# Kernel optimization log

Measured on AMD Instinct MI355X. Metric: run time of the kernel, lower is better.

The kernel has to match this reference:

```python
import jax, jax.numpy as jnp
import numpy as np
import math

D = 768; H = 12; DH = 64; LAT = 512; B = 2; L = 1024


def _rms(x, w, eps=1e-6):
    return w * x * jax.lax.rsqrt(jnp.mean(x * x, axis=-1, keepdims=True) + eps)


def _rope_tables(seq_len, dh):
    inv = 1.0 / (10000.0 ** (np.arange(0, dh, 2, dtype=np.float32) / dh))
    t = np.arange(seq_len, dtype=np.float32)
    f = np.outer(t, inv)
    emb = np.concatenate([f, f], axis=-1)
    return jnp.asarray(np.cos(emb))[None, :, None, :], jnp.asarray(np.sin(emb))[None, :, None, :]


def _rope(x, cos, sin):
    x1, x2 = jnp.split(x, 2, axis=-1)
    return x * cos + jnp.concatenate([-x2, x1], axis=-1) * sin


def setup_inputs():
    key = jax.random.key(0)
    ks = jax.random.split(key, 8)
    s = 0.02
    return {
        'x': jax.random.normal(ks[0], (B, L, D), jnp.float32),
        'w_ln': jnp.ones((D,), jnp.float32),
        'w_compress': jax.random.normal(ks[1], (D, LAT), jnp.float32) * s,
        'w_qkv': jax.random.normal(ks[2], (LAT, 3 * D), jnp.float32) * s,
        'w_reso': jax.random.normal(ks[3], (LAT, H * 4), jnp.float32) * s,
        'w_qn': jnp.ones((DH,), jnp.float32),
        'w_kn': jnp.ones((DH,), jnp.float32),
        'head_decay': jnp.linspace(-3.0, 1.0, H).astype(jnp.float32),
        'temperature': jnp.ones((1,), jnp.float32) * 0.5,
        'w_out_gate': jax.random.normal(ks[4], (LAT, D), jnp.float32) * s,
        'w_proj': jax.random.normal(ks[5], (D, D), jnp.float32) * s,
        'w_memnorm': jnp.ones((D,), jnp.float32),
    }


def reference(x, w_ln, w_compress, w_qkv, w_reso, w_qn, w_kn, head_decay, temperature, w_out_gate, w_proj, w_memnorm):
    cos, sin = _rope_tables(L, DH)
    xn = _rms(x, w_ln)
    latent = jax.nn.silu(xn @ w_compress)                        # (B,L,LAT)
    q, k, v = jnp.split(latent @ w_qkv, 3, axis=-1)
    q = _rope(_rms(q.reshape(B, L, H, DH), w_qn), cos, sin)
    k = _rope(_rms(k.reshape(B, L, H, DH), w_kn), cos, sin)
    v_f = v.reshape(B, L, H, DH)
    q_f = jax.nn.elu(q) + 1.0
    k_f = jax.nn.elu(k) + 1.0
    params = (latent @ w_reso).reshape(B, L, H, 4)
    sem_amp, sem_phase, ctx_amp, ctx_phase = [params[..., i] for i in range(4)]
    sem_phase = jax.nn.sigmoid(sem_phase) * math.pi
    ctx_phase = jax.nn.sigmoid(ctx_phase) * math.pi
    decay = jnp.clip(0.3 + 0.65 * jax.nn.sigmoid(head_decay), 1e-5, 0.999)   # (H,)
    gate = jnp.clip(jax.nn.sigmoid(jax.nn.sigmoid(sem_amp) * jax.nn.sigmoid(ctx_amp)
                                   * jnp.cos(sem_phase - ctx_phase) * temperature[0]) * 1.2 - 0.1,
                    0.05, 0.95)                                  # (B,L,H)
    one_m = (1.0 - decay)[None, None, :]                          # (1,1,H)
    kv_in = jnp.einsum('blhd,blhe->blhde', k_f, v_f) * gate[..., None, None] * one_m[..., None, None]
    z_in = k_f * one_m[..., None]
    # cumulative log-decay -> df, same as torch cumsum of constant per-step log_decay
    cum_log = jnp.arange(1, L + 1, dtype=jnp.float32)[:, None] * jnp.log(decay)[None, :]
    df = jnp.exp(cum_log)[None, :, :, None]                       # (1,L,H,1)
    kv_states = jnp.cumsum(kv_in / (df[..., None] + 1e-8), axis=1) * df[..., None]
    z_states = jnp.cumsum(z_in / (df + 1e-8), axis=1) * df
    out_num = jnp.einsum('blhd,blhde->blhe', q_f, kv_states)
    den = jnp.clip(jnp.sum(q_f * z_states, axis=-1, keepdims=True), 1e-5, None)
    out = (out_num / den).reshape(B, L, D)
    return (_rms(out, w_memnorm) @ w_proj) * jax.nn.silu(latent @ w_out_gate)
```

## Files before the change

kernel.cpp:

```cpp
#include <hip/hip_runtime.h>
#include <hip/hip_bf16.h>
#include <math.h>

#define D_MODEL 768
#define NHEAD   12
#define LATD    512
#define BATCH   2
#define SEQ     1024
#define NROWS   (BATCH*SEQ)
#define NCHUNK  (SEQ/64)
#define NBH     (BATCH*NHEAD)
#define NFUSE   3200
#define PQ      72

using short8 = __attribute__((ext_vector_type(8))) short;
using f32x4  = __attribute__((ext_vector_type(4))) float;

__device__ __forceinline__ float sigf(float x){ return 1.f/(1.f+expf(-x)); }
__device__ __forceinline__ float decay_of(float hd){
  float d = 0.3f + 0.65f*sigf(hd);
  return fminf(fmaxf(d, 1e-5f), 0.999f);
}
__device__ __forceinline__ unsigned short f2b(float f){
  __hip_bfloat16 h = __float2bfloat16(f);
  return *reinterpret_cast<unsigned short*>(&h);
}
__device__ __forceinline__ float bf2f(unsigned short u){
  unsigned int x = ((unsigned int)u) << 16;
  return __uint_as_float(x);
}
__device__ __forceinline__ void async16(const unsigned short* g, unsigned short* l){
  __builtin_amdgcn_global_load_lds((const __attribute__((address_space(1))) void*)g,
                                   (__attribute__((address_space(3))) void*)l, 16, 0, 0);
}

__global__ __launch_bounds__(256) void k_rmsnorm_bf(const float* __restrict__ x,
    const float* __restrict__ w, unsigned short* __restrict__ y)
{
  int row = blockIdx.x, tid = threadIdx.x;
  const float* xr = x + (size_t)row*D_MODEL;
  float v0 = xr[tid], v1 = xr[tid+256], v2 = xr[tid+512];
  float s = v0*v0 + v1*v1 + v2*v2;
  #pragma unroll
  for (int off=32; off; off>>=1) s += __shfl_xor(s, off, 64);
  __shared__ float red[4];
  if ((tid & 63) == 0) red[tid>>6] = s;
  __syncthreads();
  s = red[0]+red[1]+red[2]+red[3];
  float sc = rsqrtf(s*(1.f/(float)D_MODEL) + 1e-6f);
  unsigned short* yr = y + (size_t)row*D_MODEL;
  yr[tid]     = f2b(v0*sc*w[tid]);
  yr[tid+256] = f2b(v1*sc*w[tid+256]);
  yr[tid+512] = f2b(v2*sc*w[tid+512]);
}

__global__ __launch_bounds__(256) void k_cvt_all(const float* __restrict__ wc,
    const float* __restrict__ wq, const float* __restrict__ wr,
    const float* __restrict__ wg, const float* __restrict__ wp,
    unsigned short* __restrict__ wtc, unsigned short* __restrict__ wtq,
    unsigned short* __restrict__ wtg, unsigned short* __restrict__ wtp)
{
  __shared__ unsigned short tile[64][65];
  int blk = blockIdx.x, t = threadIdx.x;
  const float* W; unsigned short* WT; int K, N, bx, by;
  if (blk < 96){ W=wc; WT=wtc; K=768; N=512; bx=blk&7; by=blk>>3; }
  else if (blk < 384){ int i=blk-96;  W=wq; WT=wtq; K=512; N=2304; bx=i%36; by=i/36; }
  else if (blk < 480){ int i=blk-384; W=wg; WT=wtg; K=512; N=768;  bx=i%12; by=i/12; }
  else if (blk < 624){ int i=blk-480; W=wp; WT=wtp; K=768; N=768;  bx=i%12; by=i/12; }
  else {
    int i = blk - 624;
    #pragma unroll
    for (int j=0;j<16;j++){
      int e = i*4096 + t + j*256;
      int n = 2304 + (e >> 9), k = e & 511;
      float v = (n < 2352) ? wr[(size_t)k*48 + (n-2304)] : 0.f;
      wtq[(size_t)n*512 + k] = f2b(v);
    }
    return;
  }
  int k0 = by*64, n0 = bx*64, cr = t >> 6, cc = t & 63;
  #pragma unroll
  for (int i=0;i<16;i++){
    int r = cr + i*4;
    tile[r][cc] = f2b(W[(size_t)(k0+r)*N + n0 + cc]);
  }
  __syncthreads();
  #pragma unroll
  for (int i=0;i<16;i++){
    int nn = cr + i*4;
    WT[(size_t)(n0+nn)*K + k0 + cc] = tile[cc][nn];
  }
}

__global__ __launch_bounds__(256) void k_mfma_gemm(const unsigned short* __restrict__ A,
    const unsigned short* __restrict__ BT, float* __restrict__ Cf,
    unsigned short* __restrict__ Cb, const unsigned short* __restrict__ auxb,
    int M, int N, int K, int act)
{
  __shared__ unsigned short As[128*64];
  __shared__ unsigned short Bs[128*64];
  int tid = threadIdx.x;
  int w = tid >> 6, lane = tid & 63;
  int wm = (w >> 1)*64, wn = (w & 1)*64;
  int m16 = lane & 15, quad = lane >> 4;
  int bm = blockIdx.y*128, bn = blockIdx.x*128;

  f32x4 acc[4][4];
  #pragma unroll
  for (int i=0;i<4;i++)
    #pragma unroll
    for (int j=0;j<4;j++) acc[i][j] = (f32x4){0.f,0.f,0.f,0.f};

  for (int kk = 0; kk < K; kk += 64){
    #pragma unroll
    for (int i=0;i<4;i++){
      int g = (w*4 + i)*64 + lane;
      int m = g >> 3, c = (g & 7) ^ (m & 7);
      async16(A  + (size_t)(bm+m)*K + kk + c*8, As + (w*4+i)*512);
      async16(BT + (size_t)(bn+m)*K + kk + c*8, Bs + (w*4+i)*512);
    }
    __syncthreads();
    #pragma unroll
    for (int s=0;s<2;s++){
      short8 af[4], bf[4];
      #pragma unroll
      for (int mt=0;mt<4;mt++){
        int m = wm + mt*16 + m16;
        int idx = m*8 + ((s*4 + quad) ^ (m & 7));
        af[mt] = *(const short8*)(As + idx*8);
      }
      #pragma unroll
      for (int nt=0;nt<4;nt++){
        int n = wn + nt*16 + m16;
        int idx = n*8 + ((s*4 + quad) ^ (n & 7));
        bf[nt] = *(const short8*)(Bs + idx*8);
      }
      #pragma unroll
      for (int mt=0;mt<4;mt++)
        #pragma unroll
        for (int nt=0;nt<4;nt++)
          acc[mt][nt] = __builtin_amdgcn_mfma_f32_16x16x32_bf16(af[mt], bf[nt], acc[mt][nt], 0, 0, 0);
    }
    __syncthreads();
  }
  #pragma unroll
  for (int mt=0;mt<4;mt++){
    #pragma unroll
    for (int r=0;r<4;r++){
      int row = bm + wm + mt*16 + quad*4 + r;
      #pragma unroll
      for (int nt=0;nt<4;nt++){
        int col = bn + wn + nt*16 + m16;
        float v = acc[mt][nt][r];
        if (act == 1) v = v/(1.f + __expf(-v));
        else if (act == 2) v *= bf2f(auxb[(size_t)row*N + col]);
        if (Cf) Cf[(size_t)row*N + col] = v;
        if (Cb) Cb[(size_t)row*N + col] = f2b(v);
      }
    }
  }
}

__global__ __launch_bounds__(256) void k_gemm_fused(const unsigned short* __restrict__ A,
    const unsigned short* __restrict__ BT, const float* __restrict__ w_qn,
    const float* __restrict__ w_kn, unsigned short* __restrict__ qf,
    unsigned short* __restrict__ kf, unsigned short* __restrict__ vf,
    float* __restrict__ params, unsigned short* __restrict__ gateb)
{
  __shared__ unsigned short As[128*64];
  __shared__ unsigned short Bs[128*64];
  const int K = LATD, N = NFUSE;
  int tid = threadIdx.x;
  int w = tid >> 6, lane = tid & 63;
  int wm = (w >> 1)*64, wn = (w & 1)*64;
  int m16 = lane & 15, quad = lane >> 4;
  int bm = blockIdx.y*128, bn = blockIdx.x*128;

  f32x4 acc[4][4];
  #pragma unroll
  for (int i=0;i<4;i++)
    #pragma unroll
    for (int j=0;j<4;j++) acc[i][j] = (f32x4){0.f,0.f,0.f,0.f};

  for (int kk = 0; kk < K; kk += 64){
    #pragma unroll
    for (int i=0;i<4;i++){
      int g = (w*4 + i)*64 + lane;
      int m = g >> 3, c = (g & 7) ^ (m & 7);
      async16(A  + (size_t)(bm+m)*K + kk + c*8, As + (w*4+i)*512);
      async16(BT + (size_t)(bn+m)*K + kk + c*8, Bs + (w*4+i)*512);
    }
    __syncthreads();
    #pragma unroll
    for (int s=0;s<2;s++){
      short8 af[4], bf[4];
      #pragma unroll
      for (int mt=0;mt<4;mt++){
        int m = wm + mt*16 + m16;
        int idx = m*8 + ((s*4 + quad) ^ (m & 7));
        af[mt] = *(const short8*)(As + idx*8);
      }
      #pragma unroll
      for (int nt=0;nt<4;nt++){
        int n = wn + nt*16 + m16;
        int idx = n*8 + ((s*4 + quad) ^ (n & 7));
        bf[nt] = *(const short8*)(Bs + idx*8);
      }
      #pragma unroll
      for (int mt=0;mt<4;mt++)
        #pragma unroll
        for (int nt=0;nt<4;nt++)
          acc[mt][nt] = __builtin_amdgcn_mfma_f32_16x16x32_bf16(af[mt], bf[nt], acc[mt][nt], 0, 0, 0);
    }
    __syncthreads();
  }

  int colbase = bn + wn;
  if (colbase < 2304){
    int sec = colbase >= 1536 ? 2 : (colbase >= 768 ? 1 : 0);
    int h = (colbase - sec*768) >> 6;
    if (sec == 2){
      #pragma unroll
      for (int mt=0;mt<4;mt++)
        #pragma unroll
        for (int r=0;r<4;r++){
          int row = bm + wm + mt*16 + quad*4 + r;
          int b = row >> 10, t = row & 1023;
          size_t ob = (((size_t)(b*NHEAD+h))*SEQ + t)*64;
          #pragma unroll
          for (int nt=0;nt<4;nt++)
            vf[ob + nt*16 + m16] = f2b(acc[mt][nt][r]);
        }
    } else {
      const float* wnp = sec ? w_kn : w_qn;
      unsigned short* of = sec ? kf : qf;
      float wv4[4];
      #pragma unroll
      for (int nt=0;nt<4;nt++) wv4[nt] = wnp[nt*16 + m16];
      float inv0 = exp2f(-(float)m16*(1.f/32.f)*13.28771237954945f);
      float inv1 = inv0 * 0.01f;
      #pragma unroll
      for (int mt=0;mt<4;mt++)
        #pragma unroll
        for (int r=0;r<4;r++){
          int row = bm + wm + mt*16 + quad*4 + r;
          int b = row >> 10, t = row & 1023;
          float s = 0.f;
          #pragma unroll
          for (int nt=0;nt<4;nt++) s += acc[mt][nt][r]*acc[mt][nt][r];
          s += __shfl_xor(s, 1, 64); s += __shfl_xor(s, 2, 64);
          s += __shfl_xor(s, 4, 64); s += __shfl_xor(s, 8, 64);
          float rs = rsqrtf(s*(1.f/64.f) + 1e-6f);
          float qv[4];
          #pragma unroll
          for (int nt=0;nt<4;nt++) qv[nt] = acc[mt][nt][r]*rs*wv4[nt];
          float s0,c0,s1,c1;
          __sincosf((float)t*inv0, &s0, &c0);
          __sincosf((float)t*inv1, &s1, &c1);
          size_t ob = (((size_t)(b*NHEAD+h))*SEQ + t)*64;
          #pragma unroll
          for (int nt=0;nt<4;nt++){
            float rot = (nt < 2) ? -qv[nt+2] : qv[nt-2];
            float cs = (nt & 1) ? c1 : c0, sn = (nt & 1) ? s1 : s0;
            float val = qv[nt]*cs + rot*sn;
            val = (val > 0.f) ? val + 1.f : __expf(val);
            of[ob + nt*16 + m16] = f2b(val);
          }
        }
    }
  } else if (colbase < 2432){
    #pragma unroll
    for (int mt=0;mt<4;mt++)
      #pragma unroll
      for (int r=0;r<4;r++){
        int row = bm + wm + mt*16 + quad*4 + r;
        #pragma unroll
        for (int nt=0;nt<4;nt++){
          int p = colbase + nt*16 + m16 - 2304;
          if (p < 48) params[(size_t)row*48 + p] = acc[mt][nt][r];
        }
      }
  } else {
    #pragma unroll
    for (int mt=0;mt<4;mt++)
      #pragma unroll
      for (int r=0;r<4;r++){
        int row = bm + wm + mt*16 + quad*4 + r;
        #pragma unroll
        for (int nt=0;nt<4;nt++){
          int gc = colbase + nt*16 + m16 - 2432;
          float v = acc[mt][nt][r];
          v = v/(1.f + __expf(-v));
          gateb[(size_t)row*D_MODEL + gc] = f2b(v);
        }
      }
  }
}

__global__ __launch_bounds__(256) void k_coef(const float* __restrict__ params,
    const float* __restrict__ hdec, const float* __restrict__ temp,
    float* __restrict__ cKV, float* __restrict__ cG)
{
  int idx = blockIdx.x*256 + threadIdx.x;
  int row = idx / NHEAD, h = idx % NHEAD;
  int b = row >> 10, t = row & 1023;
  const float* pr = params + (size_t)row*48 + h*4;
  float sa = sigf(pr[0]);
  float sp = sigf(pr[1])*3.14159265358979323846f;
  float ca = sigf(pr[2]);
  float cp = sigf(pr[3])*3.14159265358979323846f;
  float z = sa*ca*cosf(sp - cp)*temp[0];
  float gate = fminf(fmaxf(sigf(z)*1.2f - 0.1f, 0.05f), 0.95f);
  float d = decay_of(hdec[h]);
  float df = expf((float)(t+1)*logf(d));
  float g = df/(df + 1e-8f);
  int ci = (b*NHEAD + h)*SEQ + t;
  cKV[ci] = g*gate*(1.f - d);
  cG[ci]  = 1.f/gate;
}

__global__ __launch_bounds__(256) void k_intra(const unsigned short* __restrict__ qf,
    const unsigned short* __restrict__ kf, const unsigned short* __restrict__ vf,
    const float* __restrict__ cKVb, const float* __restrict__ cGb,
    const float* __restrict__ hdec, float* __restrict__ numb,
    float* __restrict__ denb, float* __restrict__ Pb, float* __restrict__ zPb)
{
  __shared__ __align__(16) unsigned short Qb[64*PQ];
  __shared__ __align__(16) unsigned short Kb[64*PQ];
  __shared__ __align__(16) unsigned short KtS[64*PQ];
  __shared__ __align__(16) unsigned short Wb[64*PQ];
  __shared__ __align__(16) unsigned short Vt[80*PQ];
  __shared__ float cn[64], cps[64];
  int bid = blockIdx.x;
  int chunk = bid & 15, bh = bid >> 4, h = bh % NHEAD;
  int tid = threadIdx.x, w = tid >> 6, lane = tid & 63;
  int m16 = lane & 15, quad = lane >> 4;
  size_t base = ((size_t)bh*SEQ + chunk*64)*64;
  float d = decay_of(hdec[h]);
  float l2d = log2f(d);

  if (tid < 64){
    float c = cKVb[bh*SEQ + chunk*64 + tid];
    float pw = exp2f((float)(63 - tid)*l2d);
    cn[tid] = c;
    cps[tid] = c*pw;
    Vt[64*PQ + tid] = f2b(cGb[bh*SEQ + chunk*64 + tid]);
  }
  for (int i = tid; i < 15*PQ; i += 256) Vt[65*PQ + i] = 0;
  __syncthreads();

  #pragma unroll
  for (int i=0;i<2;i++){
    int g = tid + i*256;
    int r = g >> 3, c8 = (g & 7)*8;
    *(short8*)(Qb + r*PQ + c8) = *(const short8*)(qf + base + r*64 + c8);
    *(short8*)(Kb + r*PQ + c8) = *(const short8*)(kf + base + r*64 + c8);
  }
  {
    int s = tid & 63;
    float cpss = cps[s];
    #pragma unroll
    for (int i=0;i<2;i++){
      int c8 = ((tid >> 6) + i*4)*8;
      short8 vv = *(const short8*)(vf + base + s*64 + c8);
      short8 kk = *(const short8*)(kf + base + s*64 + c8);
      #pragma unroll
      for (int j=0;j<8;j++){
        Vt[(c8+j)*PQ + s] = ((unsigned short*)&vv)[j];
        KtS[(c8+j)*PQ + s] = f2b(bf2f(((unsigned short*)&kk)[j])*cpss);
      }
    }
  }
  __syncthreads();

  int trow = w*16 + quad*4;
  for (int stile=0; stile<4; stile++){
    if (stile > w){
      #pragma unroll
      for (int r=0;r<4;r++) Wb[(trow+r)*PQ + stile*16 + m16] = 0;
      continue;
    }
    f32x4 acc = (f32x4){0.f,0.f,0.f,0.f};
    #pragma unroll
    for (int ks=0;ks<2;ks++){
      short8 a = *(const short8*)(Qb + (w*16 + m16)*PQ + ks*32 + quad*8);
      short8 b = *(const short8*)(Kb + (stile*16 + m16)*PQ + ks*32 + quad*8);
      acc = __builtin_amdgcn_mfma_f32_16x16x32_bf16(a, b, acc, 0, 0, 0);
    }
    int s = stile*16 + m16;
    float cns = cn[s];
    #pragma unroll
    for (int r=0;r<4;r++){
      int t = trow + r;
      float wv = 0.f;
      if (s <= t) wv = acc[r]*exp2f((float)(t-s)*l2d)*cns;
      Wb[t*PQ + s] = f2b(wv);
    }
  }
  __syncthreads();

  {
    f32x4 acc[5];
    #pragma unroll
    for (int et=0;et<5;et++) acc[et] = (f32x4){0.f,0.f,0.f,0.f};
    #pragma unroll
    for (int et=0;et<5;et++)
      #pragma unroll
      for (int ks=0;ks<2;ks++){
        short8 a = *(const short8*)(Wb + (w*16 + m16)*PQ + ks*32 + quad*8);
        short8 b = *(const short8*)(Vt + (et*16 + m16)*PQ + ks*32 + quad*8);
        acc[et] = __builtin_amdgcn_mfma_f32_16x16x32_bf16(a, b, acc[et], 0, 0, 0);
      }
    #pragma unroll
    for (int et=0;et<4;et++)
      #pragma unroll
      for (int r=0;r<4;r++)
        numb[base + (size_t)(trow+r)*64 + et*16 + m16] = acc[et][r];
    if (m16 == 0){
      #pragma unroll
      for (int r=0;r<4;r++)
        denb[bh*SEQ + chunk*64 + trow + r] = acc[4][r];
    }
  }
  {
    #pragma unroll
    for (int j=0;j<5;j++){
      int tIdx = w + 4*j;
      int et = tIdx >> 2, dt = tIdx & 3;
      f32x4 acc = (f32x4){0.f,0.f,0.f,0.f};
      #pragma unroll
      for (int ks=0;ks<2;ks++){
        short8 a = *(const short8*)(Vt  + (et*16 + m16)*PQ + ks*32 + quad*8);
        short8 b = *(const short8*)(KtS + (dt*16 + m16)*PQ + ks*32 + quad*8);
        acc = __builtin_amdgcn_mfma_f32_16x16x32_bf16(a, b, acc, 0, 0, 0);
      }
      if (et < 4){
        #pragma unroll
        for (int r=0;r<4;r++)
          Pb[(size_t)bid*4096 + (et*16 + quad*4 + r)*64 + dt*16 + m16] = acc[r];
      } else {
        if (quad == 0) zPb[bid*64 + dt*16 + m16] = acc[0];
      }
    }
  }
}

__global__ __launch_bounds__(256) void k_scan(const float* __restrict__ Pb,
    const float* __restrict__ zPb, unsigned short* __restrict__ Sprev,
    unsigned short* __restrict__ zprev, const float* __restrict__ hdec)
{
  int bh = blockIdx.x >> 2, part = blockIdx.x & 3;
  int h = bh % NHEAD, tid = threadIdx.x;
  float d = decay_of(hdec[h]);
  float d64 = exp2f(64.f*log2f(d));
  int idx = part*1024 + tid*4;
  float4 S = make_float4(0.f,0.f,0.f,0.f);
  for (int c=0;c<NCHUNK;c++){
    size_t off = ((size_t)bh*NCHUNK + c)*4096 + idx;
    unsigned int lo = (unsigned int)f2b(S.x) | ((unsigned int)f2b(S.y) << 16);
    unsigned int hi = (unsigned int)f2b(S.z) | ((unsigned int)f2b(S.w) << 16);
    *(uint2*)(Sprev + off) = make_uint2(lo, hi);
    float4 p = *(const float4*)(Pb + off);
    S.x = S.x*d64 + p.x; S.y = S.y*d64 + p.y;
    S.z = S.z*d64 + p.z; S.w = S.w*d64 + p.w;
  }
  if (part == 0 && tid < 64){
    float z = 0.f;
    for (int c=0;c<NCHUNK;c++){
      int zoff = (bh*NCHUNK + c)*64 + tid;
      zprev[zoff] = f2b(z);
      z = z*d64 + zPb[zoff];
    }
  }
}

__global__ __launch_bounds__(256) void k_cross(const unsigned short* __restrict__ qf,
    const unsigned short* __restrict__ Sprev, const unsigned short* __restrict__ zprev,
    const float* __restrict__ numb, const float* __restrict__ denb,
    const float* __restrict__ hdec, float* __restrict__ attn)
{
  __shared__ __align__(16) unsigned short Qb[64*PQ];
  __shared__ __align__(16) unsigned short Sp[80*PQ];
  __shared__ float den_sm[64];
  int bid = blockIdx.x;
  int chunk = bid & 15, bh = bid >> 4, h = bh % NHEAD, b = bh / NHEAD;
  int tid = threadIdx.x, w = tid >> 6, lane = tid & 63;
  int m16 = lane & 15, quad = lane >> 4;
  size_t base = ((size_t)bh*SEQ + chunk*64)*64;
  float d = decay_of(hdec[h]);
  float l2d = log2f(d);

  #pragma unroll
  for (int i=0;i<2;i++){
    int g = tid + i*256;
    int r = g >> 3, c8 = (g & 7)*8;
    *(short8*)(Qb + r*PQ + c8) = *(const short8*)(qf + base + r*64 + c8);
    *(short8*)(Sp + r*PQ + c8) = *(const short8*)(Sprev + (size_t)bid*4096 + r*64 + c8);
  }
  if (tid < 64) Sp[64*PQ + tid] = zprev[bid*64 + tid];
  for (int i = tid; i < 15*PQ; i += 256) Sp[65*PQ + i] = 0;
  __syncthreads();

  f32x4 acc[5];
  #pragma unroll
  for (int et=0;et<5;et++) acc[et] = (f32x4){0.f,0.f,0.f,0.f};
  #pragma unroll
  for (int et=0;et<5;et++)
    #pragma unroll
    for (int ks=0;ks<2;ks++){
      short8 a = *(const short8*)(Qb + (w*16 + m16)*PQ + ks*32 + quad*8);
      short8 b = *(const short8*)(Sp + (et*16 + m16)*PQ + ks*32 + quad*8);
      acc[et] = __builtin_amdgcn_mfma_f32_16x16x32_bf16(a, b, acc[et], 0, 0, 0);
    }
  int trow = w*16 + quad*4;
  if (m16 == 0){
    #pragma unroll
    for (int r=0;r<4;r++){
      int tl = trow + r;
      float pw = exp2f((float)(tl+1)*l2d);
      float den = fmaxf(denb[bh*SEQ + chunk*64 + tl] + pw*acc[4][r], 1e-5f);
      den_sm[tl] = 1.f/den;
    }
  }
  __syncthreads();
  #pragma unroll
  for (int r=0;r<4;r++){
    int tl = trow + r;
    float pw = exp2f((float)(tl+1)*l2d);
    float invden = den_sm[tl];
    int tg = chunk*64 + tl;
    #pragma unroll
    for (int et=0;et<4;et++){
      int e = et*16 + m16;
      float nm = numb[base + (size_t)tl*64 + e] + pw*acc[et][r];
      attn[((size_t)(b*SEQ + tg))*D_MODEL + h*64 + e] = nm*invden;
    }
  }
}

extern "C" void kernel_launch(void* const* d_in, const int* in_sizes, int n_in,
                              void* d_out, int out_size, void* d_ws, size_t ws_size,
                              hipStream_t stream)
{
  (void)in_sizes; (void)n_in; (void)out_size; (void)ws_size;
  const float* x       = (const float*)d_in[0];
  const float* w_ln    = (const float*)d_in[1];
  const float* w_comp  = (const float*)d_in[2];
  const float* w_qkv   = (const float*)d_in[3];
  const float* w_reso  = (const float*)d_in[4];
  const float* w_qn    = (const float*)d_in[5];
  const float* w_kn    = (const float*)d_in[6];
  const float* hdec    = (const float*)d_in[7];
  const float* temp    = (const float*)d_in[8];
  const float* w_ogate = (const float*)d_in[9];
  const float* w_proj  = (const float*)d_in[10];
  const float* w_mn    = (const float*)d_in[11];
  float* ws = (float*)d_ws;
  float* out = (float*)d_out;

  const size_t o_params = 0;
  const size_t o_cKV    = o_params + (size_t)NROWS*48;
  const size_t o_cG     = o_cKV    + (size_t)NBH*SEQ;
  const size_t o_den    = o_cG     + (size_t)NBH*SEQ;
  const size_t o_P      = o_den    + (size_t)NBH*SEQ;
  const size_t o_zP     = o_P      + (size_t)NBH*NCHUNK*4096;
  const size_t o_attn   = o_zP     + (size_t)NBH*NCHUNK*64;
  const size_t o_numb   = o_attn   + (size_t)NROWS*D_MODEL;
  const size_t o_end    = o_numb   + (size_t)NBH*SEQ*64;

  unsigned short* bws = (unsigned short*)(ws + o_end);
  const size_t u_xn     = 0;
  const size_t u_latent = u_xn     + (size_t)NROWS*D_MODEL;
  const size_t u_memn   = u_latent + (size_t)NROWS*LATD;
  const size_t u_q      = u_memn   + (size_t)NROWS*D_MODEL;
  const size_t u_k      = u_q      + (size_t)NBH*SEQ*64;
  const size_t u_v      = u_k      + (size_t)NBH*SEQ*64;
  const size_t u_gate   = u_v      + (size_t)NBH*SEQ*64;
  const size_t u_S      = u_gate   + (size_t)NROWS*D_MODEL;
  const size_t u_zprev  = u_S      + (size_t)NBH*NCHUNK*4096;
  const size_t u_wtc    = u_zprev  + (size_t)NBH*NCHUNK*64;
  const size_t u_wtq    = u_wtc    + (size_t)LATD*D_MODEL;
  const size_t u_wtg    = u_wtq    + (size_t)2432*LATD;
  const size_t u_wtp    = u_wtg    + (size_t)D_MODEL*LATD;

  k_cvt_all<<<640, 256, 0, stream>>>(w_comp, w_qkv, w_reso, w_ogate, w_proj,
      bws + u_wtc, bws + u_wtq, bws + u_wtg, bws + u_wtp);
  k_rmsnorm_bf<<<NROWS, 256, 0, stream>>>(x, w_ln, bws + u_xn);
  k_mfma_gemm<<<dim3(LATD/128, NROWS/128), 256, 0, stream>>>(bws + u_xn, bws + u_wtc,
      nullptr, bws + u_latent, nullptr, NROWS, LATD, D_MODEL, 1);
  k_gemm_fused<<<dim3(NFUSE/128, NROWS/128), 256, 0, stream>>>(bws + u_latent, bws + u_wtq,
      w_qn, w_kn, bws + u_q, bws + u_k, bws + u_v, ws + o_params, bws + u_gate);
  k_coef<<<NROWS*NHEAD/256, 256, 0, stream>>>(ws + o_params, hdec, temp, ws + o_cKV, ws + o_cG);
  k_intra<<<NBH*NCHUNK, 256, 0, stream>>>(bws + u_q, bws + u_k, bws + u_v,
      ws + o_cKV, ws + o_cG, hdec, ws + o_numb, ws + o_den, ws + o_P, ws + o_zP);
  k_scan<<<NBH*4, 256, 0, stream>>>(ws + o_P, ws + o_zP, bws + u_S, bws + u_zprev, hdec);
  k_cross<<<NBH*NCHUNK, 256, 0, stream>>>(bws + u_q, bws + u_S, bws + u_zprev,
      ws + o_numb, ws + o_den, hdec, ws + o_attn);
  k_rmsnorm_bf<<<NROWS, 256, 0, stream>>>(ws + o_attn, w_mn, bws + u_memn);
  k_mfma_gemm<<<dim3(D_MODEL/128, NROWS/128), 256, 0, stream>>>(bws + u_memn, bws + u_wtp,
      out, nullptr, bws + u_gate, NROWS, D_MODEL, D_MODEL, 2);
}
```

Baseline: 182.7 us.

## Fuse attention stages into cooperative kernel and fold norms and coefficients into neighbors

Merges the intra-chunk, scan, cross-chunk and output RMSnorm stages into one cooperative kernel separated by grid-wide syncs. The gate and decay coefficient math moves into the fused QKV GEMM epilogue, and the input RMSnorm joins the weight-convert launch. The generic GEMM tile is narrowed to 128x64 so more blocks cover the small GEMMs. This cuts launch count and intermediate traffic, but grid.sync barriers and a scan phase using only 96 of 384 blocks serialize some work.

```diff
diff --git a/kernel.cpp b/kernel.cpp
--- a/kernel.cpp
+++ b/kernel.cpp
@@ -1,6 +1,9 @@
 #include <hip/hip_runtime.h>
 #include <hip/hip_bf16.h>
+#include <hip/hip_cooperative_groups.h>
 #include <math.h>
+
+namespace cg = cooperative_groups;
 
 #define D_MODEL 768
 #define NHEAD   12
@@ -12,6 +15,7 @@
 #define NBH     (BATCH*NHEAD)
 #define NFUSE   3200
 #define PQ      72
+#define NATTN   (NBH*NCHUNK)
 
 using short8 = __attribute__((ext_vector_type(8))) short;
 using f32x4  = __attribute__((ext_vector_type(4))) float;
@@ -34,40 +38,35 @@
                                    (__attribute__((address_space(3))) void*)l, 16, 0, 0);
 }
 
-__global__ __launch_bounds__(256) void k_rmsnorm_bf(const float* __restrict__ x,
-    const float* __restrict__ w, unsigned short* __restrict__ y)
-{
-  int row = blockIdx.x, tid = threadIdx.x;
-  const float* xr = x + (size_t)row*D_MODEL;
-  float v0 = xr[tid], v1 = xr[tid+256], v2 = xr[tid+512];
-  float s = v0*v0 + v1*v1 + v2*v2;
-  #pragma unroll
-  for (int off=32; off; off>>=1) s += __shfl_xor(s, off, 64);
-  __shared__ float red[4];
-  if ((tid & 63) == 0) red[tid>>6] = s;
-  __syncthreads();
-  s = red[0]+red[1]+red[2]+red[3];
-  float sc = rsqrtf(s*(1.f/(float)D_MODEL) + 1e-6f);
-  unsigned short* yr = y + (size_t)row*D_MODEL;
-  yr[tid]     = f2b(v0*sc*w[tid]);
-  yr[tid+256] = f2b(v1*sc*w[tid+256]);
-  yr[tid+512] = f2b(v2*sc*w[tid+512]);
-}
-
 __global__ __launch_bounds__(256) void k_cvt_all(const float* __restrict__ wc,
     const float* __restrict__ wq, const float* __restrict__ wr,
     const float* __restrict__ wg, const float* __restrict__ wp,
+    const float* __restrict__ x, const float* __restrict__ wln,
     unsigned short* __restrict__ wtc, unsigned short* __restrict__ wtq,
-    unsigned short* __restrict__ wtg, unsigned short* __restrict__ wtp)
+    unsigned short* __restrict__ wtg, unsigned short* __restrict__ wtp,
+    unsigned short* __restrict__ xn)
 {
   __shared__ unsigned short tile[64][65];
+  __shared__ float red[4];
   int blk = blockIdx.x, t = threadIdx.x;
-  const float* W; unsigned short* WT; int K, N, bx, by;
-  if (blk < 96){ W=wc; WT=wtc; K=768; N=512; bx=blk&7; by=blk>>3; }
-  else if (blk < 384){ int i=blk-96;  W=wq; WT=wtq; K=512; N=2304; bx=i%36; by=i/36; }
-  else if (blk < 480){ int i=blk-384; W=wg; WT=wtg; K=512; N=768;  bx=i%12; by=i/12; }
-  else if (blk < 624){ int i=blk-480; W=wp; WT=wtp; K=768; N=768;  bx=i%12; by=i/12; }
-  else {
+  if (blk >= 640){
+    int row = blk - 640;
+    const float* xr = x + (size_t)row*D_MODEL;
+    float v0 = xr[t], v1 = xr[t+256], v2 = xr[t+512];
+    float s = v0*v0 + v1*v1 + v2*v2;
+    #pragma unroll
+    for (int off=32; off; off>>=1) s += __shfl_xor(s, off, 64);
+    if ((t & 63) == 0) red[t>>6] = s;
+    __syncthreads();
+    s = red[0]+red[1]+red[2]+red[3];
+    float sc = rsqrtf(s*(1.f/(float)D_MODEL) + 1e-6f);
+    unsigned short* yr = xn + (size_t)row*D_MODEL;
+    yr[t]     = f2b(v0*sc*wln[t]);
+    yr[t+256] = f2b(v1*sc*wln[t+256]);
+    yr[t+512] = f2b(v2*sc*wln[t+512]);
+    return;
+  }
+  if (blk >= 624){
     int i = blk - 624;
     #pragma unroll
     for (int j=0;j<16;j++){
@@ -78,6 +77,11 @@
     }
     return;
   }
+  const float* W; unsigned short* WT; int K, N, bx, by;
+  if (blk < 96){ W=wc; WT=wtc; K=768; N=512; bx=blk&7; by=blk>>3; }
+  else if (blk < 384){ int i=blk-96;  W=wq; WT=wtq; K=512; N=2304; bx=i%36; by=i/36; }
+  else if (blk < 480){ int i=blk-384; W=wg; WT=wtg; K=512; N=768;  bx=i%12; by=i/12; }
+  else               { int i=blk-480; W=wp; WT=wtp; K=768; N=768;  bx=i%12; by=i/12; }
   int k0 = by*64, n0 = bx*64, cr = t >> 6, cc = t & 63;
   #pragma unroll
   for (int i=0;i<16;i++){
@@ -98,31 +102,36 @@
     int M, int N, int K, int act)
 {
   __shared__ unsigned short As[128*64];
-  __shared__ unsigned short Bs[128*64];
+  __shared__ unsigned short Bs[64*64];
   int tid = threadIdx.x;
   int w = tid >> 6, lane = tid & 63;
-  int wm = (w >> 1)*64, wn = (w & 1)*64;
+  int wm = (w >> 1)*64, wn = (w & 1)*32;
   int m16 = lane & 15, quad = lane >> 4;
-  int bm = blockIdx.y*128, bn = blockIdx.x*128;
-
-  f32x4 acc[4][4];
+  int bm = blockIdx.y*128, bn = blockIdx.x*64;
+
+  f32x4 acc[4][2];
   #pragma unroll
   for (int i=0;i<4;i++)
     #pragma unroll
-    for (int j=0;j<4;j++) acc[i][j] = (f32x4){0.f,0.f,0.f,0.f};
+    for (int j=0;j<2;j++) acc[i][j] = (f32x4){0.f,0.f,0.f,0.f};
 
   for (int kk = 0; kk < K; kk += 64){
     #pragma unroll
     for (int i=0;i<4;i++){
       int g = (w*4 + i)*64 + lane;
       int m = g >> 3, c = (g & 7) ^ (m & 7);
-      async16(A  + (size_t)(bm+m)*K + kk + c*8, As + (w*4+i)*512);
-      async16(BT + (size_t)(bn+m)*K + kk + c*8, Bs + (w*4+i)*512);
+      async16(A + (size_t)(bm+m)*K + kk + c*8, As + (w*4+i)*512);
+    }
+    #pragma unroll
+    for (int i=0;i<2;i++){
+      int g = (w*2 + i)*64 + lane;
+      int m = g >> 3, c = (g & 7) ^ (m & 7);
+      async16(BT + (size_t)(bn+m)*K + kk + c*8, Bs + (w*2+i)*512);
     }
     __syncthreads();
     #pragma unroll
     for (int s=0;s<2;s++){
-      short8 af[4], bf[4];
+      short8 af[4], bf[2];
       #pragma unroll
       for (int mt=0;mt<4;mt++){
         int m = wm + mt*16 + m16;
@@ -130,7 +139,7 @@
         af[mt] = *(const short8*)(As + idx*8);
       }
       #pragma unroll
-      for (int nt=0;nt<4;nt++){
+      for (int nt=0;nt<2;nt++){
         int n = wn + nt*16 + m16;
         int idx = n*8 + ((s*4 + quad) ^ (n & 7));
         bf[nt] = *(const short8*)(Bs + idx*8);
@@ -138,7 +147,7 @@
       #pragma unroll
       for (int mt=0;mt<4;mt++)
         #pragma unroll
-        for (int nt=0;nt<4;nt++)
+        for (int nt=0;nt<2;nt++)
           acc[mt][nt] = __builtin_amdgcn_mfma_f32_16x16x32_bf16(af[mt], bf[nt], acc[mt][nt], 0, 0, 0);
     }
     __syncthreads();
@@ -149,7 +158,7 @@
     for (int r=0;r<4;r++){
       int row = bm + wm + mt*16 + quad*4 + r;
       #pragma unroll
-      for (int nt=0;nt<4;nt++){
+      for (int nt=0;nt<2;nt++){
         int col = bn + wn + nt*16 + m16;
         float v = acc[mt][nt][r];
         if (act == 1) v = v/(1.f + __expf(-v));
@@ -163,13 +172,15 @@
 
 __global__ __launch_bounds__(256) void k_gemm_fused(const unsigned short* __restrict__ A,
     const unsigned short* __restrict__ BT, const float* __restrict__ w_qn,
-    const float* __restrict__ w_kn, unsigned short* __restrict__ qf,
+    const float* __restrict__ w_kn, const float* __restrict__ hdec,
+    const float* __restrict__ temp, unsigned short* __restrict__ qf,
     unsigned short* __restrict__ kf, unsigned short* __restrict__ vf,
-    float* __restrict__ params, unsigned short* __restrict__ gateb)
+    float* __restrict__ cKV, float* __restrict__ cG,
+    unsigned short* __restrict__ gateb)
 {
   __shared__ unsigned short As[128*64];
   __shared__ unsigned short Bs[128*64];
-  const int K = LATD, N = NFUSE;
+  const int K = LATD;
   int tid = threadIdx.x;
   int w = tid >> 6, lane = tid & 63;
   int wm = (w >> 1)*64, wn = (w & 1)*64;
@@ -268,19 +279,38 @@
           }
         }
     }
-  } else if (colbase < 2432){
+  } else if (colbase == 2304){
+    float temp0 = temp[0];
     #pragma unroll
     for (int mt=0;mt<4;mt++)
       #pragma unroll
       for (int r=0;r<4;r++){
         int row = bm + wm + mt*16 + quad*4 + r;
-        #pragma unroll
-        for (int nt=0;nt<4;nt++){
-          int p = colbase + nt*16 + m16 - 2304;
-          if (p < 48) params[(size_t)row*48 + p] = acc[mt][nt][r];
-        }
-      }
-  } else {
+        int b = row >> 10, t = row & 1023;
+        #pragma unroll
+        for (int nt=0;nt<3;nt++){
+          int p = nt*16 + m16, h2 = p >> 2, pi = p & 3;
+          float v  = acc[mt][nt][r];
+          float v1 = __shfl_xor(v, 1, 64);
+          float v2 = __shfl_xor(v, 2, 64);
+          float v3 = __shfl_xor(v, 3, 64);
+          if (pi == 0){
+            float sa = sigf(v);
+            float sp = sigf(v1)*3.14159265358979323846f;
+            float ca = sigf(v2);
+            float cp = sigf(v3)*3.14159265358979323846f;
+            float z = sa*ca*cosf(sp - cp)*temp0;
+            float gate = fminf(fmaxf(sigf(z)*1.2f - 0.1f, 0.05f), 0.95f);
+            float dd = decay_of(hdec[h2]);
+            float df = expf((float)(t+1)*logf(dd));
+            float g = df/(df + 1e-8f);
+            int ci = (b*NHEAD + h2)*SEQ + t;
+            cKV[ci] = g*gate*(1.f - dd);
+            cG[ci]  = 1.f/gate;
+          }
+        }
+      }
+  } else if (colbase >= 2432){
     #pragma unroll
     for (int mt=0;mt<4;mt++)
       #pragma unroll
@@ -297,191 +327,19 @@
   }
 }
 
-__global__ __launch_bounds__(256) void k_coef(const float* __restrict__ params,
-    const float* __restrict__ hdec, const float* __restrict__ temp,
-    float* __restrict__ cKV, float* __restrict__ cG)
+__global__ __launch_bounds__(256) void k_attn(
+    const unsigned short* __restrict__ qf, const unsigned short* __restrict__ kf,
+    const unsigned short* __restrict__ vf, const float* __restrict__ cKVb,
+    const float* __restrict__ cGb, const float* __restrict__ hdec,
+    float* __restrict__ numb, float* __restrict__ denb,
+    float* __restrict__ Pb, float* __restrict__ zPb,
+    unsigned short* __restrict__ Sprev, unsigned short* __restrict__ zprev,
+    float* __restrict__ attn, const float* __restrict__ w_mn,
+    unsigned short* __restrict__ memn)
 {
-  int idx = blockIdx.x*256 + threadIdx.x;
-  int row = idx / NHEAD, h = idx % NHEAD;
-  int b = row >> 10, t = row & 1023;
-  const float* pr = params + (size_t)row*48 + h*4;
-  float sa = sigf(pr[0]);
-  float sp = sigf(pr[1])*3.14159265358979323846f;
-  float ca = sigf(pr[2]);
-  float cp = sigf(pr[3])*3.14159265358979323846f;
-  float z = sa*ca*cosf(sp - cp)*temp[0];
-  float gate = fminf(fmaxf(sigf(z)*1.2f - 0.1f, 0.05f), 0.95f);
-  float d = decay_of(hdec[h]);
-  float df = expf((float)(t+1)*logf(d));
-  float g = df/(df + 1e-8f);
-  int ci = (b*NHEAD + h)*SEQ + t;
-  cKV[ci] = g*gate*(1.f - d);
-  cG[ci]  = 1.f/gate;
-}
-
-__global__ __launch_bounds__(256) void k_intra(const unsigned short* __restrict__ qf,
-    const unsigned short* __restrict__ kf, const unsigned short* __restrict__ vf,
-    const float* __restrict__ cKVb, const float* __restrict__ cGb,
-    const float* __restrict__ hdec, float* __restrict__ numb,
-    float* __restrict__ denb, float* __restrict__ Pb, float* __restrict__ zPb)
-{
-  __shared__ __align__(16) unsigned short Qb[64*PQ];
-  __shared__ __align__(16) unsigned short Kb[64*PQ];
-  __shared__ __align__(16) unsigned short KtS[64*PQ];
-  __shared__ __align__(16) unsigned short Wb[64*PQ];
-  __shared__ __align__(16) unsigned short Vt[80*PQ];
-  __shared__ float cn[64], cps[64];
-  int bid = blockIdx.x;
-  int chunk = bid & 15, bh = bid >> 4, h = bh % NHEAD;
-  int tid = threadIdx.x, w = tid >> 6, lane = tid & 63;
-  int m16 = lane & 15, quad = lane >> 4;
-  size_t base = ((size_t)bh*SEQ + chunk*64)*64;
-  float d = decay_of(hdec[h]);
-  float l2d = log2f(d);
-
-  if (tid < 64){
-    float c = cKVb[bh*SEQ + chunk*64 + tid];
-    float pw = exp2f((float)(63 - tid)*l2d);
-    cn[tid] = c;
-    cps[tid] = c*pw;
-    Vt[64*PQ + tid] = f2b(cGb[bh*SEQ + chunk*64 + tid]);
-  }
-  for (int i = tid; i < 15*PQ; i += 256) Vt[65*PQ + i] = 0;
-  __syncthreads();
-
-  #pragma unroll
-  for (int i=0;i<2;i++){
-    int g = tid + i*256;
-    int r = g >> 3, c8 = (g & 7)*8;
-    *(short8*)(Qb + r*PQ + c8) = *(const short8*)(qf + base + r*64 + c8);
-    *(short8*)(Kb + r*PQ + c8) = *(const short8*)(kf + base + r*64 + c8);
-  }
-  {
-    int s = tid & 63;
-    float cpss = cps[s];
-    #pragma unroll
-    for (int i=0;i<2;i++){
-      int c8 = ((tid >> 6) + i*4)*8;
-      short8 vv = *(const short8*)(vf + base + s*64 + c8);
-      short8 kk = *(const short8*)(kf + base + s*64 + c8);
-      #pragma unroll
-      for (int j=0;j<8;j++){
-        Vt[(c8+j)*PQ + s] = ((unsigned short*)&vv)[j];
-        KtS[(c8+j)*PQ + s] = f2b(bf2f(((unsigned short*)&kk)[j])*cpss);
-      }
-    }
-  }
-  __syncthreads();
-
-  int trow = w*16 + quad*4;
-  for (int stile=0; stile<4; stile++){
-    if (stile > w){
-      #pragma unroll
-      for (int r=0;r<4;r++) Wb[(trow+r)*PQ + stile*16 + m16] = 0;
-      continue;
-    }
-    f32x4 acc = (f32x4){0.f,0.f,0.f,0.f};
-    #pragma unroll
-    for (int ks=0;ks<2;ks++){
-      short8 a = *(const short8*)(Qb + (w*16 + m16)*PQ + ks*32 + quad*8);
-      short8 b = *(const short8*)(Kb + (stile*16 + m16)*PQ + ks*32 + quad*8);
-      acc = __builtin_amdgcn_mfma_f32_16x16x32_bf16(a, b, acc, 0, 0, 0);
-    }
-    int s = stile*16 + m16;
-    float cns = cn[s];
-    #pragma unroll
-    for (int r=0;r<4;r++){
-      int t = trow + r;
-      float wv = 0.f;
-      if (s <= t) wv = acc[r]*exp2f((float)(t-s)*l2d)*cns;
-      Wb[t*PQ + s] = f2b(wv);
-    }
-  }
-  __syncthreads();
-
-  {
-    f32x4 acc[5];
-    #pragma unroll
-    for (int et=0;et<5;et++) acc[et] = (f32x4){0.f,0.f,0.f,0.f};
-    #pragma unroll
-    for (int et=0;et<5;et++)
-      #pragma unroll
-      for (int ks=0;ks<2;ks++){
-        short8 a = *(const short8*)(Wb + (w*16 + m16)*PQ + ks*32 + quad*8);
-        short8 b = *(const short8*)(Vt + (et*16 + m16)*PQ + ks*32 + quad*8);
-        acc[et] = __builtin_amdgcn_mfma_f32_16x16x32_bf16(a, b, acc[et], 0, 0, 0);
-      }
-    #pragma unroll
-    for (int et=0;et<4;et++)
-      #pragma unroll
-      for (int r=0;r<4;r++)
-        numb[base + (size_t)(trow+r)*64 + et*16 + m16] = acc[et][r];
-    if (m16 == 0){
-      #pragma unroll
-      for (int r=0;r<4;r++)
-        denb[bh*SEQ + chunk*64 + trow + r] = acc[4][r];
-    }
-  }
-  {
-    #pragma unroll
-    for (int j=0;j<5;j++){
-      int tIdx = w + 4*j;
-      int et = tIdx >> 2, dt = tIdx & 3;
-      f32x4 acc = (f32x4){0.f,0.f,0.f,0.f};
-      #pragma unroll
-      for (int ks=0;ks<2;ks++){
-        short8 a = *(const short8*)(Vt  + (et*16 + m16)*PQ + ks*32 + quad*8);
-        short8 b = *(const short8*)(KtS + (dt*16 + m16)*PQ + ks*32 + quad*8);
-        acc = __builtin_amdgcn_mfma_f32_16x16x32_bf16(a, b, acc, 0, 0, 0);
-      }
-      if (et < 4){
-        #pragma unroll
-        for (int r=0;r<4;r++)
-          Pb[(size_t)bid*4096 + (et*16 + quad*4 + r)*64 + dt*16 + m16] = acc[r];
-      } else {
-        if (quad == 0) zPb[bid*64 + dt*16 + m16] = acc[0];
-      }
-    }
-  }
-}
-
-__global__ __launch_bounds__(256) void k_scan(const float* __restrict__ Pb,
-    const float* __restrict__ zPb, unsigned short* __restrict__ Sprev,
-    unsigned short* __restrict__ zprev, const float* __restrict__ hdec)
-{
-  int bh = blockIdx.x >> 2, part = blockIdx.x & 3;
-  int h = bh % NHEAD, tid = threadIdx.x;
-  float d = decay_of(hdec[h]);
-  float d64 = exp2f(64.f*log2f(d));
-  int idx = part*1024 + tid*4;
-  float4 S = make_float4(0.f,0.f,0.f,0.f);
-  for (int c=0;c<NCHUNK;c++){
-    size_t off = ((size_t)bh*NCHUNK + c)*4096 + idx;
-    unsigned int lo = (unsigned int)f2b(S.x) | ((unsigned int)f2b(S.y) << 16);
-    unsigned int hi = (unsigned int)f2b(S.z) | ((unsigned int)f2b(S.w) << 16);
-    *(uint2*)(Sprev + off) = make_uint2(lo, hi);
-    float4 p = *(const float4*)(Pb + off);
-    S.x = S.x*d64 + p.x; S.y = S.y*d64 + p.y;
-    S.z = S.z*d64 + p.z; S.w = S.w*d64 + p.w;
-  }
-  if (part == 0 && tid < 64){
-    float z = 0.f;
-    for (int c=0;c<NCHUNK;c++){
-      int zoff = (bh*NCHUNK + c)*64 + tid;
-      zprev[zoff] = f2b(z);
-      z = z*d64 + zPb[zoff];
-    }
-  }
-}
-
-__global__ __launch_bounds__(256) void k_cross(const unsigned short* __restrict__ qf,
-    const unsigned short* __restrict__ Sprev, const unsigned short* __restrict__ zprev,
-    const float* __restrict__ numb, const float* __restrict__ denb,
-    const float* __restrict__ hdec, float* __restrict__ attn)
-{
-  __shared__ __align__(16) unsigned short Qb[64*PQ];
-  __shared__ __align__(16) unsigned short Sp[80*PQ];
-  __shared__ float den_sm[64];
+  cg::grid_group grid = cg::this_grid();
+  __shared__ __align__(16) unsigned short sm_u[336*PQ];
+  __shared__ float cn[64], cps[64], den_sm[64], red[4];
   int bid = blockIdx.x;
   int chunk = bid & 15, bh = bid >> 4, h = bh % NHEAD, b = bh / NHEAD;
   int tid = threadIdx.x, w = tid >> 6, lane = tid & 63;
@@ -490,51 +348,215 @@
   float d = decay_of(hdec[h]);
   float l2d = log2f(d);
 
-  #pragma unroll
-  for (int i=0;i<2;i++){
-    int g = tid + i*256;
-    int r = g >> 3, c8 = (g & 7)*8;
-    *(short8*)(Qb + r*PQ + c8) = *(const short8*)(qf + base + r*64 + c8);
-    *(short8*)(Sp + r*PQ + c8) = *(const short8*)(Sprev + (size_t)bid*4096 + r*64 + c8);
-  }
-  if (tid < 64) Sp[64*PQ + tid] = zprev[bid*64 + tid];
-  for (int i = tid; i < 15*PQ; i += 256) Sp[65*PQ + i] = 0;
-  __syncthreads();
-
-  f32x4 acc[5];
-  #pragma unroll
-  for (int et=0;et<5;et++) acc[et] = (f32x4){0.f,0.f,0.f,0.f};
-  #pragma unroll
-  for (int et=0;et<5;et++)
-    #pragma unroll
-    for (int ks=0;ks<2;ks++){
-      short8 a = *(const short8*)(Qb + (w*16 + m16)*PQ + ks*32 + quad*8);
-      short8 b = *(const short8*)(Sp + (et*16 + m16)*PQ + ks*32 + quad*8);
-      acc[et] = __builtin_amdgcn_mfma_f32_16x16x32_bf16(a, b, acc[et], 0, 0, 0);
-    }
-  int trow = w*16 + quad*4;
-  if (m16 == 0){
+  {
+    unsigned short* Qb  = sm_u;
+    unsigned short* Kb  = sm_u + 64*PQ;
+    unsigned short* KtS = sm_u + 128*PQ;
+    unsigned short* Wb  = sm_u + 192*PQ;
+    unsigned short* Vt  = sm_u + 256*PQ;
+
+    if (tid < 64){
+      float c = cKVb[bh*SEQ + chunk*64 + tid];
+      float pw = exp2f((float)(63 - tid)*l2d);
+      cn[tid] = c;
+      cps[tid] = c*pw;
+      Vt[64*PQ + tid] = f2b(cGb[bh*SEQ + chunk*64 + tid]);
+    }
+    for (int i = tid; i < 15*PQ; i += 256) Vt[65*PQ + i] = 0;
+    __syncthreads();
+
+    #pragma unroll
+    for (int i=0;i<2;i++){
+      int g = tid + i*256;
+      int r = g >> 3, c8 = (g & 7)*8;
+      *(short8*)(Qb + r*PQ + c8) = *(const short8*)(qf + base + r*64 + c8);
+      *(short8*)(Kb + r*PQ + c8) = *(const short8*)(kf + base + r*64 + c8);
+    }
+    {
+      int s = tid & 63;
+      float cpss = cps[s];
+      #pragma unroll
+      for (int i=0;i<2;i++){
+        int c8 = ((tid >> 6) + i*4)*8;
+        short8 vv = *(const short8*)(vf + base + s*64 + c8);
+        short8 kk = *(const short8*)(kf + base + s*64 + c8);
+        #pragma unroll
+        for (int j=0;j<8;j++){
+          Vt[(c8+j)*PQ + s] = ((unsigned short*)&vv)[j];
+          KtS[(c8+j)*PQ + s] = f2b(bf2f(((unsigned short*)&kk)[j])*cpss);
+        }
+      }
+    }
+    __syncthreads();
+
+    int trow = w*16 + quad*4;
+    for (int stile=0; stile<4; stile++){
+      if (stile > w){
+        #pragma unroll
+        for (int r=0;r<4;r++) Wb[(trow+r)*PQ + stile*16 + m16] = 0;
+        continue;
+      }
+      f32x4 acc = (f32x4){0.f,0.f,0.f,0.f};
+      #pragma unroll
+      for (int ks=0;ks<2;ks++){
+        short8 a = *(const short8*)(Qb + (w*16 + m16)*PQ + ks*32 + quad*8);
+        short8 bv = *(const short8*)(Kb + (stile*16 + m16)*PQ + ks*32 + quad*8);
+        acc = __builtin_amdgcn_mfma_f32_16x16x32_bf16(a, bv, acc, 0, 0, 0);
+      }
+      int s = stile*16 + m16;
+      float cns = cn[s];
+      #pragma unroll
+      for (int r=0;r<4;r++){
+        int t = trow + r;
+        float wv = 0.f;
+        if (s <= t) wv = acc[r]*exp2f((float)(t-s)*l2d)*cns;
+        Wb[t*PQ + s] = f2b(wv);
+      }
+    }
+    __syncthreads();
+
+    {
+      f32x4 acc[5];
+      #pragma unroll
+      for (int et=0;et<5;et++) acc[et] = (f32x4){0.f,0.f,0.f,0.f};
+      #pragma unroll
+      for (int et=0;et<5;et++)
+        #pragma unroll
+        for (int ks=0;ks<2;ks++){
+          short8 a = *(const short8*)(Wb + (w*16 + m16)*PQ + ks*32 + quad*8);
+          short8 bv = *(const short8*)(Vt + (et*16 + m16)*PQ + ks*32 + quad*8);
+          acc[et] = __builtin_amdgcn_mfma_f32_16x16x32_bf16(a, bv, acc[et], 0, 0, 0);
+        }
+      #pragma unroll
+      for (int et=0;et<4;et++)
+        #pragma unroll
+        for (int r=0;r<4;r++)
+          numb[base + (size_t)(trow+r)*64 + et*16 + m16] = acc[et][r];
+      if (m16 == 0){
+        #pragma unroll
+        for (int r=0;r<4;r++)
+          denb[bh*SEQ + chunk*64 + trow + r] = acc[4][r];
+      }
+    }
+    {
+      #pragma unroll
+      for (int j=0;j<5;j++){
+        int tIdx = w + 4*j;
+        int et = tIdx >> 2, dt = tIdx & 3;
+        f32x4 acc = (f32x4){0.f,0.f,0.f,0.f};
+        #pragma unroll
+        for (int ks=0;ks<2;ks++){
+          short8 a = *(const short8*)(Vt  + (et*16 + m16)*PQ + ks*32 + quad*8);
+          short8 bv = *(const short8*)(KtS + (dt*16 + m16)*PQ + ks*32 + quad*8);
+          acc = __builtin_amdgcn_mfma_f32_16x16x32_bf16(a, bv, acc, 0, 0, 0);
+        }
+        if (et < 4){
+          #pragma unroll
+          for (int r=0;r<4;r++)
+            Pb[(size_t)bid*4096 + (et*16 + quad*4 + r)*64 + dt*16 + m16] = acc[r];
+        } else {
+          if (quad == 0) zPb[bid*64 + dt*16 + m16] = acc[0];
+        }
+      }
+    }
+  }
+  __threadfence();
+  grid.sync();
+
+  if (bid < 96){
+    int bh2 = bid >> 2, part = bid & 3, h2 = bh2 % NHEAD;
+    float d2 = decay_of(hdec[h2]);
+    float d64 = exp2f(64.f*log2f(d2));
+    int idx = part*1024 + tid*4;
+    float4 S = make_float4(0.f,0.f,0.f,0.f);
+    for (int c=0;c<NCHUNK;c++){
+      size_t off = ((size_t)bh2*NCHUNK + c)*4096 + idx;
+      unsigned int lo = (unsigned int)f2b(S.x) | ((unsigned int)f2b(S.y) << 16);
+      unsigned int hi = (unsigned int)f2b(S.z) | ((unsigned int)f2b(S.w) << 16);
+      *(uint2*)(Sprev + off) = make_uint2(lo, hi);
+      float4 p = *(const float4*)(Pb + off);
+      S.x = S.x*d64 + p.x; S.y = S.y*d64 + p.y;
+      S.z = S.z*d64 + p.z; S.w = S.w*d64 + p.w;
+    }
+    if (part == 0 && tid < 64){
+      float z = 0.f;
+      for (int c=0;c<NCHUNK;c++){
+        int zoff = (bh2*NCHUNK + c)*64 + tid;
+        zprev[zoff] = f2b(z);
+        z = z*d64 + zPb[zoff];
+      }
+    }
+  }
+  __threadfence();
+  grid.sync();
+
+  {
+    unsigned short* Qb = sm_u;
+    unsigned short* Sp = sm_u + 64*PQ;
+    #pragma unroll
+    for (int i=0;i<2;i++){
+      int g = tid + i*256;
+      int r = g >> 3, c8 = (g & 7)*8;
+      *(short8*)(Sp + r*PQ + c8) = *(const short8*)(Sprev + (size_t)bid*4096 + r*64 + c8);
+    }
+    if (tid < 64) Sp[64*PQ + tid] = zprev[bid*64 + tid];
+    for (int i = tid; i < 15*PQ; i += 256) Sp[65*PQ + i] = 0;
+    __syncthreads();
+
+    f32x4 acc[5];
+    #pragma unroll
+    for (int et=0;et<5;et++) acc[et] = (f32x4){0.f,0.f,0.f,0.f};
+    #pragma unroll
+    for (int et=0;et<5;et++)
+      #pragma unroll
+      for (int ks=0;ks<2;ks++){
+        short8 a = *(const short8*)(Qb + (w*16 + m16)*PQ + ks*32 + quad*8);
+        short8 bv = *(const short8*)(Sp + (et*16 + m16)*PQ + ks*32 + quad*8);
+        acc[et] = __builtin_amdgcn_mfma_f32_16x16x32_bf16(a, bv, acc[et], 0, 0, 0);
+      }
+    int trow = w*16 + quad*4;
+    if (m16 == 0){
+      #pragma unroll
+      for (int r=0;r<4;r++){
+        int tl = trow + r;
+        float pw = exp2f((float)(tl+1)*l2d);
+        float den = fmaxf(denb[bh*SEQ + chunk*64 + tl] + pw*acc[4][r], 1e-5f);
+        den_sm[tl] = 1.f/den;
+      }
+    }
+    __syncthreads();
     #pragma unroll
     for (int r=0;r<4;r++){
       int tl = trow + r;
       float pw = exp2f((float)(tl+1)*l2d);
-      float den = fmaxf(denb[bh*SEQ + chunk*64 + tl] + pw*acc[4][r], 1e-5f);
-      den_sm[tl] = 1.f/den;
-    }
-  }
-  __syncthreads();
-  #pragma unroll
-  for (int r=0;r<4;r++){
-    int tl = trow + r;
-    float pw = exp2f((float)(tl+1)*l2d);
-    float invden = den_sm[tl];
-    int tg = chunk*64 + tl;
-    #pragma unroll
-    for (int et=0;et<4;et++){
-      int e = et*16 + m16;
-      float nm = numb[base + (size_t)tl*64 + e] + pw*acc[et][r];
-      attn[((size_t)(b*SEQ + tg))*D_MODEL + h*64 + e] = nm*invden;
-    }
+      float invden = den_sm[tl];
+      int tg = chunk*64 + tl;
+      #pragma unroll
+      for (int et=0;et<4;et++){
+        int e = et*16 + m16;
+        float nm = numb[base + (size_t)tl*64 + e] + pw*acc[et][r];
+        attn[((size_t)(b*SEQ + tg))*D_MODEL + h*64 + e] = nm*invden;
+      }
+    }
+  }
+  __threadfence();
+  grid.sync();
+
+  for (int row = bid; row < NROWS; row += NATTN){
+    const float* xr = attn + (size_t)row*D_MODEL;
+    float v0 = xr[tid], v1 = xr[tid+256], v2 = xr[tid+512];
+    float s = v0*v0 + v1*v1 + v2*v2;
+    #pragma unroll
+    for (int off=32; off; off>>=1) s += __shfl_xor(s, off, 64);
+    if ((tid & 63) == 0) red[tid>>6] = s;
+    __syncthreads();
+    s = red[0]+red[1]+red[2]+red[3];
+    float sc = rsqrtf(s*(1.f/(float)D_MODEL) + 1e-6f);
+    unsigned short* yr = memn + (size_t)row*D_MODEL;
+    yr[tid]     = f2b(v0*sc*w_mn[tid]);
+    yr[tid+256] = f2b(v1*sc*w_mn[tid+256]);
+    yr[tid+512] = f2b(v2*sc*w_mn[tid+512]);
+    __syncthreads();
   }
 }
 
@@ -558,8 +580,7 @@
   float* ws = (float*)d_ws;
   float* out = (float*)d_out;
 
-  const size_t o_params = 0;
-  const size_t o_cKV    = o_params + (size_t)NROWS*48;
+  const size_t o_cKV    = 0;
   const size_t o_cG     = o_cKV    + (size_t)NBH*SEQ;
   const size_t o_den    = o_cG     + (size_t)NBH*SEQ;
   const size_t o_P      = o_den    + (size_t)NBH*SEQ;
@@ -583,20 +604,34 @@
   const size_t u_wtg    = u_wtq    + (size_t)2432*LATD;
   const size_t u_wtp    = u_wtg    + (size_t)D_MODEL*LATD;
 
-  k_cvt_all<<<640, 256, 0, stream>>>(w_comp, w_qkv, w_reso, w_ogate, w_proj,
-      bws + u_wtc, bws + u_wtq, bws + u_wtg, bws + u_wtp);
-  k_rmsnorm_bf<<<NROWS, 256, 0, stream>>>(x, w_ln, bws + u_xn);
-  k_mfma_gemm<<<dim3(LATD/128, NROWS/128), 256, 0, stream>>>(bws + u_xn, bws + u_wtc,
+  k_cvt_all<<<2688, 256, 0, stream>>>(w_comp, w_qkv, w_reso, w_ogate, w_proj,
+      x, w_ln, bws + u_wtc, bws + u_wtq, bws + u_wtg, bws + u_wtp, bws + u_xn);
+  k_mfma_gemm<<<dim3(LATD/64, NROWS/128), 256, 0, stream>>>(bws + u_xn, bws + u_wtc,
       nullptr, bws + u_latent, nullptr, NROWS, LATD, D_MODEL, 1);
   k_gemm_fused<<<dim3(NFUSE/128, NROWS/128), 256, 0, stream>>>(bws + u_latent, bws + u_wtq,
-      w_qn, w_kn, bws + u_q, bws + u_k, bws + u_v, ws + o_params, bws + u_gate);
-  k_coef<<<NROWS*NHEAD/256, 256, 0, stream>>>(ws + o_params, hdec, temp, ws + o_cKV, ws + o_cG);
-  k_intra<<<NBH*NCHUNK, 256, 0, stream>>>(bws + u_q, bws + u_k, bws + u_v,
-      ws + o_cKV, ws + o_cG, hdec, ws + o_numb, ws + o_den, ws + o_P, ws + o_zP);
-  k_scan<<<NBH*4, 256, 0, stream>>>(ws + o_P, ws + o_zP, bws + u_S, bws + u_zprev, hdec);
-  k_cross<<<NBH*NCHUNK, 256, 0, stream>>>(bws + u_q, bws + u_S, bws + u_zprev,
-      ws + o_numb, ws + o_den, hdec, ws + o_attn);
-  k_rmsnorm_bf<<<NROWS, 256, 0, stream>>>(ws + o_attn, w_mn, bws + u_memn);
-  k_mfma_gemm<<<dim3(D_MODEL/128, NROWS/128), 256, 0, stream>>>(bws + u_memn, bws + u_wtp,
+      w_qn, w_kn, hdec, temp, bws + u_q, bws + u_k, bws + u_v,
+      ws + o_cKV, ws + o_cG, bws + u_gate);
+  {
+    const unsigned short* a_qf = bws + u_q;
+    const unsigned short* a_kf = bws + u_k;
+    const unsigned short* a_vf = bws + u_v;
+    const float* a_cKV = ws + o_cKV;
+    const float* a_cG  = ws + o_cG;
+    const float* a_hd  = hdec;
+    float* a_numb = ws + o_numb;
+    float* a_den  = ws + o_den;
+    float* a_P    = ws + o_P;
+    float* a_zP   = ws + o_zP;
+    unsigned short* a_S  = bws + u_S;
+    unsigned short* a_zp = bws + u_zprev;
+    float* a_attn = ws + o_attn;
+    const float* a_wmn = w_mn;
+    unsigned short* a_memn = bws + u_memn;
+    void* kargs[] = { &a_qf, &a_kf, &a_vf, &a_cKV, &a_cG, &a_hd, &a_numb, &a_den,
+                      &a_P, &a_zP, &a_S, &a_zp, &a_attn, &a_wmn, &a_memn };
+    hipLaunchCooperativeKernel((const void*)k_attn, dim3(NATTN), dim3(256),
+                               kargs, 0, stream);
+  }
+  k_mfma_gemm<<<dim3(D_MODEL/64, NROWS/128), 256, 0, stream>>>(bws + u_memn, bws + u_wtp,
       out, nullptr, bws + u_gate, NROWS, D_MODEL, D_MODEL, 2);
 }
```

Result: slower. 519.5 us (+184.3%).
